# Optimization experiments

Measured on AMD Instinct MI355X. Metric: run time of the kernel, lower is better.

Reference implementation:

```python
import jax, jax.numpy as jnp
import numpy as np

B, S, E, H, L, NQ, FFN, V, C = 16, 2048, 256, 4, 2, 8, 512, 50257, 2
DK = E // H  # wires per attention head


def _pos_encoding(seq_len, dim):
    pos = jnp.arange(seq_len, dtype=jnp.float32)[:, None]
    div = jnp.exp(jnp.arange(0, dim, 2, dtype=jnp.float32) * (-np.log(10000.0) / dim))
    pe = jnp.zeros((seq_len, dim), dtype=jnp.float32)
    pe = pe.at[:, 0::2].set(jnp.sin(pos * div))
    pe = pe.at[:, 1::2].set(jnp.cos(pos * div))
    return pe


def _layernorm(x, g, b, eps=1e-5):
    m = x.mean(-1, keepdims=True)
    v = ((x - m) ** 2).mean(-1, keepdims=True)
    return (x - m) / jnp.sqrt(v + eps) * g + b


def setup_inputs() -> dict:
    key = jax.random.key(0)
    ks = jax.random.split(key, 9)
    f = lambda k, shape, s: jax.random.normal(k, shape, dtype=jnp.float32) * s
    return {
        "tokens": jax.random.randint(ks[0], (B, S), 0, V),
        "embed": f(ks[1], (V, E), 0.02),
        "attn_theta": f(ks[2], (L, DK), 1.0),
        "combine_w": f(ks[3], (L, E, E), 0.05),
        "combine_b": jnp.zeros((L, E), jnp.float32),
        "ffn_theta": f(ks[4], (L, NQ), 1.0),
        "lin1_w": f(ks[5], (L, NQ, FFN), 0.1),
        "lin1_b": jnp.zeros((L, FFN), jnp.float32),
        "lin2_w": f(ks[6], (L, FFN, E), 0.05),
        "lin2_b": jnp.zeros((L, E), jnp.float32),
        "ln1_g": jnp.ones((L, E), jnp.float32),
        "ln1_b": jnp.zeros((L, E), jnp.float32),
        "ln2_g": jnp.ones((L, E), jnp.float32),
        "ln2_b": jnp.zeros((L, E), jnp.float32),
        "cls_w": f(ks[7], (E, C), 0.05),
        "cls_b": jnp.zeros((C,), jnp.float32),
    }


def reference(tokens, embed, attn_theta, combine_w, combine_b, ffn_theta,
              lin1_w, lin1_b, lin2_w, lin2_b, ln1_g, ln1_b, ln2_g, ln2_b,
              cls_w, cls_b):
    # token embedding + sinusoidal positional encoding
    x = embed[tokens] + _pos_encoding(S, E)[None]  # [B,S,E]
    for l in range(L):
        # QuantumAttention: per-head RX-encode(x) then trainable RX(theta),
        # PauliZ expectation => cos(x + theta); same theta shared across heads,
        # head split/merge preserves feature layout => tile theta over heads.
        theta = jnp.tile(attn_theta[l], H)  # [E]
        attn = jnp.einsum('bse,ef->bsf', jnp.cos(x + theta), combine_w[l]) + combine_b[l]
        x = _layernorm(x + attn, ln1_g[l], ln1_b[l])
        # FeedForwardQuantum: RX-encode first NQ features, trainable RY(theta),
        # PauliZ expectation => cos(x) * cos(theta)
        q = jnp.cos(x[..., :NQ]) * jnp.cos(ffn_theta[l])  # [B,S,NQ]
        h = jax.nn.relu(jnp.einsum('bsn,nf->bsf', q, lin1_w[l]) + lin1_b[l])
        ffn = jnp.einsum('bsf,fe->bse', h, lin2_w[l]) + lin2_b[l]
        x = _layernorm(x + ffn, ln2_g[l], ln2_b[l])
    pooled = x.mean(axis=1)  # [B,E]
    return pooled @ cls_w + cls_b  # [B,C] logits
```

## Files before the change

kernel.cpp:

```cpp
#include <hip/hip_runtime.h>
#include <cstdint>
#include <cstddef>

#define SEQ   2048
#define EDIM  256
#define FFND  512
#define NBATCH 16
#define XLD   264

typedef unsigned short u16;
typedef __attribute__((ext_vector_type(8))) __bf16 bf16x8;
typedef __attribute__((ext_vector_type(4))) float f32x4;

__device__ __forceinline__ float bf2f(u16 u) {
  union { unsigned int w; float f; } v; v.w = ((unsigned int)u) << 16; return v.f;
}
__device__ __forceinline__ u16 f2bf(float f) {
  union { float f; unsigned int w; } v; v.f = f;
  unsigned int r = v.w + 0x7fffu + ((v.w >> 16) & 1u);
  return (u16)(r >> 16);
}
__device__ __forceinline__ float fast_cos(float x) {
  float r = x * 0.15915494309189535f;
  r = r - floorf(r);
  return __builtin_amdgcn_cosf(r);
}
__device__ __forceinline__ void unpack8(bf16x8 v, float* o) {
  const u16* p = (const u16*)&v;
  #pragma unroll
  for (int j = 0; j < 8; ++j) o[j] = bf2f(p[j]);
}

__global__ void sniff_kernel(const void* embed, int* flag) {
  int t = threadIdx.x;
  const u16* p = (const u16*)embed;
  int c = 0;
  #pragma unroll
  for (int j = 0; j < 8; ++j) {
    u16 v = p[t * 8 + j];
    int e = (v >> 7) & 0xff;
    c += (e > 128) ? 1 : 0;
  }
  #pragma unroll
  for (int d = 1; d < 64; d <<= 1) c += __shfl_xor(c, d);
  if (t == 0) *flag = (c > 64) ? 1 : 0;
}

struct CanonArgs { const void* p[14]; };

__global__ void canon_kernel(CanonArgs a, const int* __restrict__ flag, u16* __restrict__ dst) {
  const int off[15] = {0, 128, 131200, 131712, 131728, 139920, 140944, 403088,
                       403600, 404112, 404624, 405136, 405648, 406160, 406162};
  int i = blockIdx.x * 256 + threadIdx.x;
  if (i >= 406162) return;
  int isf32 = *flag;
  int s = 0;
  #pragma unroll
  for (int k = 0; k < 13; ++k) s += (i >= off[k + 1]) ? 1 : 0;
  int j = i - off[s];
  u16 v = isf32 ? f2bf(((const float*)a.p[s])[j]) : ((const u16*)a.p[s])[j];
  dst[i] = v;
}

__global__ void prep_kernel(const u16* __restrict__ cw, const u16* __restrict__ l2,
                            u16* __restrict__ cwT, u16* __restrict__ l2T) {
  int id = blockIdx.x * 256 + threadIdx.x;
  if (id < 2 * 256 * 256) {
    int l = id >> 16, rem = id & 65535;
    int kc = rem >> 11, n = (rem >> 3) & 255, kj = rem & 7;
    cwT[id] = cw[l * 65536 + (kc * 8 + kj) * 256 + n];
  } else {
    int j = id - 131072;
    if (j < 2 * 512 * 256) {
      int l = j >> 17, rem = j & 131071;
      int kc = rem >> 11, n = (rem >> 3) & 255, kj = rem & 7;
      l2T[j] = l2[l * 131072 + (kc * 8 + kj) * 256 + n];
    }
  }
}

__launch_bounds__(256, 2)
__global__ void mega_kernel(const int* __restrict__ tokens, const void* __restrict__ embed,
                            const int* __restrict__ flag, const u16* __restrict__ canon,
                            const u16* __restrict__ cwT, const u16* __restrict__ l2T,
                            float* __restrict__ pooled) {
  __shared__ u16 xt[64 * XLD];
  __shared__ union {
    struct { u16 Bt[256 * 64]; u16 At[64 * 64]; u16 qs[64 * 8]; } k;
    struct { float2 sstat[64][5]; float2 sms[64]; } ln;
  } sh;
  __shared__ u16 thL[64];

  const int tid = threadIdx.x;
  const int wave = tid >> 6, lane = tid & 63;
  const int fr = lane & 15, fq = lane >> 4;
  const int m0 = blockIdx.x * 64;
  const int isf32 = *flag;

  int cols[4];
  #pragma unroll
  for (int ni = 0; ni < 4; ++ni) cols[ni] = wave * 64 + ni * 16 + fr;

  {
    const float c0 = 9.210340371976184f / 128.f;
    const float inv2pi = 0.15915494309189535f;
    #pragma unroll
    for (int it = 0; it < 8; ++it) {
      int c = it * 256 + tid;
      int r = c >> 5, e8 = c & 31;
      int tok = tokens[m0 + r];
      float ev[8];
      if (isf32) {
        const float* ep = (const float*)embed + (size_t)tok * EDIM + e8 * 8;
        float4 a = *(const float4*)ep, b = *(const float4*)(ep + 4);
        ev[0]=a.x; ev[1]=a.y; ev[2]=a.z; ev[3]=a.w; ev[4]=b.x; ev[5]=b.y; ev[6]=b.z; ev[7]=b.w;
      } else {
        const u16* ep = (const u16*)embed + (size_t)tok * EDIM + e8 * 8;
        uint4 v = *(const uint4*)ep;
        unpack8(*(const bf16x8*)&v, ev);
      }
      int s = (m0 + r) & (SEQ - 1);
      u16 o[8];
      #pragma unroll
      for (int j = 0; j < 8; ++j) {
        int e = e8 * 8 + j, i = e >> 1;
        float rev = (float)s * (__expf(-(float)i * c0) * inv2pi);
        rev = rev - floorf(rev);
        float pe = (e & 1) ? __builtin_amdgcn_cosf(rev) : __builtin_amdgcn_sinf(rev);
        o[j] = f2bf(ev[j] + pe);
      }
      *(uint4*)(xt + r * XLD + e8 * 8) = *(const uint4*)o;
    }
  }
  __syncthreads();

  f32x4 acc[4][4];

  auto mfma_step = [&]() {
    const bf16x8* Av = (const bf16x8*)sh.k.At;
    const bf16x8* Bv = (const bf16x8*)sh.k.Bt;
    #pragma unroll
    for (int ks = 0; ks < 2; ++ks) {
      const int kc = ks * 4 + fq;
      bf16x8 af[4], bfv[4];
      #pragma unroll
      for (int mi = 0; mi < 4; ++mi) af[mi] = Av[kc * 64 + ((mi * 16 + fr) ^ kc)];
      #pragma unroll
      for (int ni = 0; ni < 4; ++ni) bfv[ni] = Bv[kc * 256 + cols[ni]];
      #pragma unroll
      for (int mi = 0; mi < 4; ++mi)
        #pragma unroll
        for (int ni = 0; ni < 4; ++ni)
          acc[mi][ni] = __builtin_amdgcn_mfma_f32_16x16x32_bf16(af[mi], bfv[ni], acc[mi][ni], 0, 0, 0);
    }
  };

  auto epilogue = [&](const u16* bias, const u16* gamma, const u16* beta) {
    float bcol[4];
    #pragma unroll
    for (int ni = 0; ni < 4; ++ni) bcol[ni] = bf2f(bias[cols[ni]]);
    #pragma unroll
    for (int mi = 0; mi < 4; ++mi)
      #pragma unroll
      for (int rg = 0; rg < 4; ++rg) {
        int lrow = mi * 16 + fq * 4 + rg;
        #pragma unroll
        for (int ni = 0; ni < 4; ++ni)
          acc[mi][ni][rg] += bf2f(xt[lrow * XLD + cols[ni]]) + bcol[ni];
      }
    float sr[4][4], sq[4][4];
    #pragma unroll
    for (int mi = 0; mi < 4; ++mi)
      #pragma unroll
      for (int rg = 0; rg < 4; ++rg) {
        float a = 0.f, b = 0.f;
        #pragma unroll
        for (int ni = 0; ni < 4; ++ni) { float t2 = acc[mi][ni][rg]; a += t2; b += t2 * t2; }
        sr[mi][rg] = a; sq[mi][rg] = b;
      }
    #pragma unroll
    for (int d = 1; d < 16; d <<= 1)
      #pragma unroll
      for (int mi = 0; mi < 4; ++mi)
        #pragma unroll
        for (int rg = 0; rg < 4; ++rg) {
          sr[mi][rg] += __shfl_xor(sr[mi][rg], d);
          sq[mi][rg] += __shfl_xor(sq[mi][rg], d);
        }
    if (fr == 0) {
      #pragma unroll
      for (int mi = 0; mi < 4; ++mi)
        #pragma unroll
        for (int rg = 0; rg < 4; ++rg)
          sh.ln.sstat[mi * 16 + fq * 4 + rg][wave] = float2{sr[mi][rg], sq[mi][rg]};
    }
    __syncthreads();
    if (tid < 64) {
      float s = 0.f, s2 = 0.f;
      #pragma unroll
      for (int w = 0; w < 4; ++w) { float2 p = sh.ln.sstat[tid][w]; s += p.x; s2 += p.y; }
      float mean = s * (1.f / 256.f);
      float var = fmaxf(s2 * (1.f / 256.f) - mean * mean, 0.f);
      sh.ln.sms[tid] = float2{mean, rsqrtf(var + 1e-5f)};
    }
    __syncthreads();
    float gcol[4], btc[4];
    #pragma unroll
    for (int ni = 0; ni < 4; ++ni) { gcol[ni] = bf2f(gamma[cols[ni]]); btc[ni] = bf2f(beta[cols[ni]]); }
    #pragma unroll
    for (int mi = 0; mi < 4; ++mi)
      #pragma unroll
      for (int rg = 0; rg < 4; ++rg) {
        int lrow = mi * 16 + fq * 4 + rg;
        float2 ms = sh.ln.sms[lrow];
        #pragma unroll
        for (int ni = 0; ni < 4; ++ni) {
          float o = (acc[mi][ni][rg] - ms.x) * ms.y * gcol[ni] + btc[ni];
          xt[lrow * XLD + cols[ni]] = f2bf(o);
        }
      }
    __syncthreads();
  };

  for (int l = 0; l < 2; ++l) {
    if (tid < 8) ((uint4*)thL)[tid] = ((const uint4*)(canon + l * 64))[tid];
    __syncthreads();
    #pragma unroll
    for (int i = 0; i < 4; ++i)
      #pragma unroll
      for (int j = 0; j < 4; ++j) acc[i][j] = {0.f, 0.f, 0.f, 0.f};
    {
      const u16* Bbase = cwT + l * 65536;
      for (int k0 = 0; k0 < 256; k0 += 64) {
        const u16* bsrc = Bbase + (k0 >> 3) * 2048;
        #pragma unroll
        for (int it = 0; it < 8; ++it) {
          int c = tid + it * 256;
          __builtin_amdgcn_global_load_lds(
              (const __attribute__((address_space(1))) void*)(bsrc + (size_t)c * 8),
              (__attribute__((address_space(3))) void*)(sh.k.Bt + c * 8), 16, 0, 0);
        }
        #pragma unroll
        for (int it = 0; it < 2; ++it) {
          int c = it * 256 + tid;
          int f8 = c >> 6, r = c & 63;
          uint4 g = *(const uint4*)(xt + r * XLD + k0 + f8 * 8);
          u16* gp = (u16*)&g;
          #pragma unroll
          for (int j = 0; j < 8; ++j)
            gp[j] = f2bf(fast_cos(bf2f(gp[j]) + bf2f(thL[f8 * 8 + j])));
          ((uint4*)sh.k.At)[f8 * 64 + (r ^ f8)] = g;
        }
        __syncthreads();
        mfma_step();
        __syncthreads();
      }
    }
    epilogue(canon + 131200 + l * 256, canon + 403600 + l * 256, canon + 404112 + l * 256);

    #pragma unroll
    for (int rep = 0; rep < 2; ++rep) {
      int idx = tid + rep * 256;
      int r = idx >> 3, n = idx & 7;
      float cth = fast_cos(bf2f(canon[131712 + l * 8 + n]));
      sh.k.qs[r * 8 + n] = f2bf(fast_cos(bf2f(xt[r * XLD + n])) * cth);
    }
    __syncthreads();

    #pragma unroll
    for (int i = 0; i < 4; ++i)
      #pragma unroll
      for (int j = 0; j < 4; ++j) acc[i][j] = {0.f, 0.f, 0.f, 0.f};
    {
      const u16* B2 = l2T + l * 131072;
      const u16* w1 = canon + 131728 + l * 4096;
      const u16* b1 = canon + 139920 + l * 512;
      for (int k0 = 0; k0 < 512; k0 += 64) {
        const u16* bsrc = B2 + (k0 >> 3) * 2048;
        #pragma unroll
        for (int it = 0; it < 8; ++it) {
          int c = tid + it * 256;
          __builtin_amdgcn_global_load_lds(
              (const __attribute__((address_space(1))) void*)(bsrc + (size_t)c * 8),
              (__attribute__((address_space(3))) void*)(sh.k.Bt + c * 8), 16, 0, 0);
        }
        #pragma unroll
        for (int it = 0; it < 2; ++it) {
          int c = it * 256 + tid;
          int kc = c >> 6, r = c & 63;
          int cc = (k0 >> 3) + kc;
          float qf[8], hv[8];
          unpack8(((const bf16x8*)sh.k.qs)[r], qf);
          { uint4 bv = *(const uint4*)(b1 + cc * 8); unpack8(*(const bf16x8*)&bv, hv); }
          #pragma unroll
          for (int n = 0; n < 8; ++n) {
            uint4 wv = *(const uint4*)(w1 + n * 512 + cc * 8);
            float wf[8];
            unpack8(*(const bf16x8*)&wv, wf);
            #pragma unroll
            for (int j = 0; j < 8; ++j) hv[j] += qf[n] * wf[j];
          }
          uint4 g; u16* gp = (u16*)&g;
          #pragma unroll
          for (int j = 0; j < 8; ++j) gp[j] = f2bf(fmaxf(hv[j], 0.f));
          ((uint4*)sh.k.At)[kc * 64 + (r ^ kc)] = g;
        }
        __syncthreads();
        mfma_step();
        __syncthreads();
      }
    }
    epilogue(canon + 403088 + l * 256, canon + 404624 + l * 256, canon + 405136 + l * 256);
  }

  {
    float s = 0.f;
    #pragma unroll 8
    for (int r = 0; r < 64; ++r) s += bf2f(xt[r * XLD + tid]);
    atomicAdd(&pooled[(m0 >> 11) * EDIM + tid], s);
  }
}

__global__ void logits_kernel(const float* __restrict__ pooled, const u16* __restrict__ clsw,
                              const u16* __restrict__ clsb, const int* __restrict__ flag,
                              void* __restrict__ out) {
  int t = threadIdx.x;
  int b = t >> 4, sub = t & 15;
  float a0 = 0.f, a1 = 0.f;
  #pragma unroll
  for (int j = 0; j < 16; ++j) {
    int e = sub * 16 + j;
    float p = pooled[b * 256 + e];
    a0 += p * bf2f(clsw[e * 2 + 0]);
    a1 += p * bf2f(clsw[e * 2 + 1]);
  }
  #pragma unroll
  for (int d = 1; d < 16; d <<= 1) {
    a0 += __shfl_xor(a0, d);
    a1 += __shfl_xor(a1, d);
  }
  if (sub == 0) {
    float o0 = a0 * (1.f / 2048.f) + bf2f(clsb[0]);
    float o1 = a1 * (1.f / 2048.f) + bf2f(clsb[1]);
    if (*flag) {
      ((float*)out)[b * 2 + 0] = o0; ((float*)out)[b * 2 + 1] = o1;
    } else {
      ((u16*)out)[b * 2 + 0] = f2bf(o0); ((u16*)out)[b * 2 + 1] = f2bf(o1);
    }
  }
}

extern "C" void kernel_launch(void* const* d_in, const int* in_sizes, int n_in,
                              void* d_out, int out_size, void* d_ws, size_t ws_size,
                              hipStream_t stream) {
  const int* tokens = (const int*)d_in[0];

  char* ws = (char*)d_ws;
  u16*   canon  = (u16*)(ws + 0);
  u16*   cwT    = (u16*)(ws + 1048576);
  u16*   l2T    = (u16*)(ws + 1310720);
  float* pooled = (float*)(ws + 1835008);
  int*   flag   = (int*)(ws + 1851392);

  sniff_kernel<<<1, 64, 0, stream>>>(d_in[1], flag);

  CanonArgs ca;
  for (int i = 0; i < 14; ++i) ca.p[i] = d_in[i + 2];
  canon_kernel<<<1587, 256, 0, stream>>>(ca, flag, canon);

  prep_kernel<<<1536, 256, 0, stream>>>(canon + 128, canon + 140944, cwT, l2T);

  hipMemsetAsync(pooled, 0, NBATCH * EDIM * sizeof(float), stream);

  mega_kernel<<<512, 256, 0, stream>>>(tokens, d_in[1], flag, canon, cwT, l2T, pooled);

  logits_kernel<<<1, 256, 0, stream>>>(pooled, canon + 405648, canon + 406160, flag, d_out);
}
```

Measured before the change: 215.4 us.

## Merge preprocessing kernels, inline dtype sniffing, use fp32 FFN weights and shared-memory LN stats

Removes the separate sniff and canon kernels. Each kernel now detects the input dtype inline, and a single prep kernel both canonicalizes the parameters and transposes the weights, cutting kernel launches and dependent passes. The FFN first layer now keeps its weights, bias and q values in fp32, which avoids bf16 unpacking in the hot loop. LayerNorm partial sums are written straight to shared memory, replacing the cross-lane shuffle reduction. The trade-offs are that every thread repeats the 128-word sniff read, there is more shared-memory traffic for the LN partials, and the fp32 weight loads are wider.

```diff
diff --git a/kernel.cpp b/kernel.cpp
--- a/kernel.cpp
+++ b/kernel.cpp
@@ -30,64 +30,64 @@
   #pragma unroll
   for (int j = 0; j < 8; ++j) o[j] = bf2f(p[j]);
 }
-
-__global__ void sniff_kernel(const void* embed, int* flag) {
-  int t = threadIdx.x;
-  const u16* p = (const u16*)embed;
+__device__ __forceinline__ int sniff128(const void* embed) {
+  const unsigned* p = (const unsigned*)embed;
   int c = 0;
   #pragma unroll
-  for (int j = 0; j < 8; ++j) {
-    u16 v = p[t * 8 + j];
-    int e = (v >> 7) & 0xff;
-    c += (e > 128) ? 1 : 0;
-  }
-  #pragma unroll
-  for (int d = 1; d < 64; d <<= 1) c += __shfl_xor(c, d);
-  if (t == 0) *flag = (c > 64) ? 1 : 0;
+  for (int j = 0; j < 128; ++j) {
+    unsigned v = p[j];
+    c += (((v >> 7) & 0xffu) > 128u) ? 1 : 0;
+    c += (((v >> 23) & 0xffu) > 128u) ? 1 : 0;
+  }
+  return c > 32;
+}
+__device__ __forceinline__ float cvt(const void* p, int j, int isf32) {
+  return isf32 ? ((const float*)p)[j] : bf2f(((const u16*)p)[j]);
 }
 
 struct CanonArgs { const void* p[14]; };
 
-__global__ void canon_kernel(CanonArgs a, const int* __restrict__ flag, u16* __restrict__ dst) {
-  const int off[15] = {0, 128, 131200, 131712, 131728, 139920, 140944, 403088,
-                       403600, 404112, 404624, 405136, 405648, 406160, 406162};
-  int i = blockIdx.x * 256 + threadIdx.x;
-  if (i >= 406162) return;
-  int isf32 = *flag;
-  int s = 0;
-  #pragma unroll
-  for (int k = 0; k < 13; ++k) s += (i >= off[k + 1]) ? 1 : 0;
-  int j = i - off[s];
-  u16 v = isf32 ? f2bf(((const float*)a.p[s])[j]) : ((const u16*)a.p[s])[j];
-  dst[i] = v;
-}
-
-__global__ void prep_kernel(const u16* __restrict__ cw, const u16* __restrict__ l2,
-                            u16* __restrict__ cwT, u16* __restrict__ l2T) {
+__global__ void prep_kernel(const void* __restrict__ emb, CanonArgs a,
+                            u16* __restrict__ canon, u16* __restrict__ cwT,
+                            u16* __restrict__ l2T, float* __restrict__ w1f,
+                            float* __restrict__ b1f) {
+  const int isf32 = sniff128(emb);
   int id = blockIdx.x * 256 + threadIdx.x;
-  if (id < 2 * 256 * 256) {
-    int l = id >> 16, rem = id & 65535;
+  if (id < 406162) {
+    const int off[15] = {0, 128, 131200, 131712, 131728, 139920, 140944, 403088,
+                         403600, 404112, 404624, 405136, 405648, 406160, 406162};
+    int s = 0;
+    #pragma unroll
+    for (int k = 0; k < 13; ++k) s += (id >= off[k + 1]) ? 1 : 0;
+    canon[id] = f2bf(cvt(a.p[s], id - off[s], isf32));
+  } else if (id < 537234) {
+    int j = id - 406162;
+    int l = j >> 16, rem = j & 65535;
     int kc = rem >> 11, n = (rem >> 3) & 255, kj = rem & 7;
-    cwT[id] = cw[l * 65536 + (kc * 8 + kj) * 256 + n];
-  } else {
-    int j = id - 131072;
-    if (j < 2 * 512 * 256) {
-      int l = j >> 17, rem = j & 131071;
-      int kc = rem >> 11, n = (rem >> 3) & 255, kj = rem & 7;
-      l2T[j] = l2[l * 131072 + (kc * 8 + kj) * 256 + n];
-    }
+    cwT[j] = f2bf(cvt(a.p[1], l * 65536 + (kc * 8 + kj) * 256 + n, isf32));
+  } else if (id < 799378) {
+    int j = id - 537234;
+    int l = j >> 17, rem = j & 131071;
+    int kc = rem >> 11, n = (rem >> 3) & 255, kj = rem & 7;
+    l2T[j] = f2bf(cvt(a.p[6], l * 131072 + (kc * 8 + kj) * 256 + n, isf32));
+  } else if (id < 807570) {
+    int j = id - 799378;
+    w1f[j] = cvt(a.p[4], j, isf32);
+  } else if (id < 808594) {
+    int j = id - 807570;
+    b1f[j] = cvt(a.p[5], j, isf32);
   }
 }
 
 __launch_bounds__(256, 2)
 __global__ void mega_kernel(const int* __restrict__ tokens, const void* __restrict__ embed,
-                            const int* __restrict__ flag, const u16* __restrict__ canon,
-                            const u16* __restrict__ cwT, const u16* __restrict__ l2T,
-                            float* __restrict__ pooled) {
+                            const u16* __restrict__ canon, const u16* __restrict__ cwT,
+                            const u16* __restrict__ l2T, const float* __restrict__ w1f,
+                            const float* __restrict__ b1f, float* __restrict__ pooled) {
   __shared__ u16 xt[64 * XLD];
   __shared__ union {
-    struct { u16 Bt[256 * 64]; u16 At[64 * 64]; u16 qs[64 * 8]; } k;
-    struct { float2 sstat[64][5]; float2 sms[64]; } ln;
+    struct { u16 Bt[256 * 64]; u16 At[64 * 64]; float qsf[64 * 8]; } k;
+    struct { float2 part[64][65]; float2 ms[64]; } ln;
   } sh;
   __shared__ u16 thL[64];
 
@@ -95,7 +95,7 @@
   const int wave = tid >> 6, lane = tid & 63;
   const int fr = lane & 15, fq = lane >> 4;
   const int m0 = blockIdx.x * 64;
-  const int isf32 = *flag;
+  const int isf32 = sniff128(embed);
 
   int cols[4];
   #pragma unroll
@@ -164,44 +164,26 @@
       #pragma unroll
       for (int rg = 0; rg < 4; ++rg) {
         int lrow = mi * 16 + fq * 4 + rg;
-        #pragma unroll
-        for (int ni = 0; ni < 4; ++ni)
-          acc[mi][ni][rg] += bf2f(xt[lrow * XLD + cols[ni]]) + bcol[ni];
-      }
-    float sr[4][4], sq[4][4];
-    #pragma unroll
-    for (int mi = 0; mi < 4; ++mi)
-      #pragma unroll
-      for (int rg = 0; rg < 4; ++rg) {
         float a = 0.f, b = 0.f;
         #pragma unroll
-        for (int ni = 0; ni < 4; ++ni) { float t2 = acc[mi][ni][rg]; a += t2; b += t2 * t2; }
-        sr[mi][rg] = a; sq[mi][rg] = b;
-      }
-    #pragma unroll
-    for (int d = 1; d < 16; d <<= 1)
-      #pragma unroll
-      for (int mi = 0; mi < 4; ++mi)
-        #pragma unroll
-        for (int rg = 0; rg < 4; ++rg) {
-          sr[mi][rg] += __shfl_xor(sr[mi][rg], d);
-          sq[mi][rg] += __shfl_xor(sq[mi][rg], d);
-        }
-    if (fr == 0) {
-      #pragma unroll
-      for (int mi = 0; mi < 4; ++mi)
-        #pragma unroll
-        for (int rg = 0; rg < 4; ++rg)
-          sh.ln.sstat[mi * 16 + fq * 4 + rg][wave] = float2{sr[mi][rg], sq[mi][rg]};
-    }
+        for (int ni = 0; ni < 4; ++ni) {
+          float t2 = acc[mi][ni][rg] + bf2f(xt[lrow * XLD + cols[ni]]) + bcol[ni];
+          acc[mi][ni][rg] = t2;
+          a += t2; b += t2 * t2;
+        }
+        sh.ln.part[lrow][wave * 16 + fr] = float2{a, b};
+      }
     __syncthreads();
     if (tid < 64) {
       float s = 0.f, s2 = 0.f;
       #pragma unroll
-      for (int w = 0; w < 4; ++w) { float2 p = sh.ln.sstat[tid][w]; s += p.x; s2 += p.y; }
+      for (int f = 0; f < 64; f += 2) {
+        float4 p = *(const float4*)&sh.ln.part[tid][f];
+        s += p.x + p.z; s2 += p.y + p.w;
+      }
       float mean = s * (1.f / 256.f);
       float var = fmaxf(s2 * (1.f / 256.f) - mean * mean, 0.f);
-      sh.ln.sms[tid] = float2{mean, rsqrtf(var + 1e-5f)};
+      sh.ln.ms[tid] = float2{mean, rsqrtf(var + 1e-5f)};
     }
     __syncthreads();
     float gcol[4], btc[4];
@@ -212,7 +194,7 @@
       #pragma unroll
       for (int rg = 0; rg < 4; ++rg) {
         int lrow = mi * 16 + fq * 4 + rg;
-        float2 ms = sh.ln.sms[lrow];
+        float2 ms = sh.ln.ms[lrow];
         #pragma unroll
         for (int ni = 0; ni < 4; ++ni) {
           float o = (acc[mi][ni][rg] - ms.x) * ms.y * gcol[ni] + btc[ni];
@@ -263,7 +245,7 @@
       int idx = tid + rep * 256;
       int r = idx >> 3, n = idx & 7;
       float cth = fast_cos(bf2f(canon[131712 + l * 8 + n]));
-      sh.k.qs[r * 8 + n] = f2bf(fast_cos(bf2f(xt[r * XLD + n])) * cth);
+      sh.k.qsf[r * 8 + n] = fast_cos(bf2f(xt[r * XLD + n])) * cth;
     }
     __syncthreads();
 
@@ -273,8 +255,8 @@
       for (int j = 0; j < 4; ++j) acc[i][j] = {0.f, 0.f, 0.f, 0.f};
     {
       const u16* B2 = l2T + l * 131072;
-      const u16* w1 = canon + 131728 + l * 4096;
-      const u16* b1 = canon + 139920 + l * 512;
+      const float* w1l = w1f + l * 4096;
+      const float* b1l = b1f + l * 512;
       for (int k0 = 0; k0 < 512; k0 += 64) {
         const u16* bsrc = B2 + (k0 >> 3) * 2048;
         #pragma unroll
@@ -289,16 +271,24 @@
           int c = it * 256 + tid;
           int kc = c >> 6, r = c & 63;
           int cc = (k0 >> 3) + kc;
-          float qf[8], hv[8];
-          unpack8(((const bf16x8*)sh.k.qs)[r], qf);
-          { uint4 bv = *(const uint4*)(b1 + cc * 8); unpack8(*(const bf16x8*)&bv, hv); }
+          float4 qa = *(const float4*)(sh.k.qsf + r * 8);
+          float4 qb = *(const float4*)(sh.k.qsf + r * 8 + 4);
+          float qv[8] = {qa.x, qa.y, qa.z, qa.w, qb.x, qb.y, qb.z, qb.w};
+          float hv[8];
+          {
+            float4 b0 = *(const float4*)(b1l + cc * 8);
+            float4 b1v = *(const float4*)(b1l + cc * 8 + 4);
+            hv[0]=b0.x; hv[1]=b0.y; hv[2]=b0.z; hv[3]=b0.w;
+            hv[4]=b1v.x; hv[5]=b1v.y; hv[6]=b1v.z; hv[7]=b1v.w;
+          }
           #pragma unroll
           for (int n = 0; n < 8; ++n) {
-            uint4 wv = *(const uint4*)(w1 + n * 512 + cc * 8);
-            float wf[8];
-            unpack8(*(const bf16x8*)&wv, wf);
-            #pragma unroll
-            for (int j = 0; j < 8; ++j) hv[j] += qf[n] * wf[j];
+            float4 w0 = *(const float4*)(w1l + n * 512 + cc * 8);
+            float4 w1v = *(const float4*)(w1l + n * 512 + cc * 8 + 4);
+            hv[0] += qv[n] * w0.x;  hv[1] += qv[n] * w0.y;
+            hv[2] += qv[n] * w0.z;  hv[3] += qv[n] * w0.w;
+            hv[4] += qv[n] * w1v.x; hv[5] += qv[n] * w1v.y;
+            hv[6] += qv[n] * w1v.z; hv[7] += qv[n] * w1v.w;
           }
           uint4 g; u16* gp = (u16*)&g;
           #pragma unroll
@@ -322,8 +312,9 @@
 }
 
 __global__ void logits_kernel(const float* __restrict__ pooled, const u16* __restrict__ clsw,
-                              const u16* __restrict__ clsb, const int* __restrict__ flag,
+                              const u16* __restrict__ clsb, const void* __restrict__ embed,
                               void* __restrict__ out) {
+  const int isf32 = sniff128(embed);
   int t = threadIdx.x;
   int b = t >> 4, sub = t & 15;
   float a0 = 0.f, a1 = 0.f;
@@ -342,7 +333,7 @@
   if (sub == 0) {
     float o0 = a0 * (1.f / 2048.f) + bf2f(clsb[0]);
     float o1 = a1 * (1.f / 2048.f) + bf2f(clsb[1]);
-    if (*flag) {
+    if (isf32) {
       ((float*)out)[b * 2 + 0] = o0; ((float*)out)[b * 2 + 1] = o1;
     } else {
       ((u16*)out)[b * 2 + 0] = f2bf(o0); ((u16*)out)[b * 2 + 1] = f2bf(o1);
@@ -359,20 +350,17 @@
   u16*   canon  = (u16*)(ws + 0);
   u16*   cwT    = (u16*)(ws + 1048576);
   u16*   l2T    = (u16*)(ws + 1310720);
-  float* pooled = (float*)(ws + 1835008);
-  int*   flag   = (int*)(ws + 1851392);
-
-  sniff_kernel<<<1, 64, 0, stream>>>(d_in[1], flag);
+  float* w1f    = (float*)(ws + 1835008);
+  float* b1f    = (float*)(ws + 1867776);
+  float* pooled = (float*)(ws + 1871872);
 
   CanonArgs ca;
   for (int i = 0; i < 14; ++i) ca.p[i] = d_in[i + 2];
-  canon_kernel<<<1587, 256, 0, stream>>>(ca, flag, canon);
-
-  prep_kernel<<<1536, 256, 0, stream>>>(canon + 128, canon + 140944, cwT, l2T);
-
+
+  prep_kernel<<<3159, 256, 0, stream>>>(d_in[1], ca, canon, cwT, l2T, w1f, b1f);
   hipMemsetAsync(pooled, 0, NBATCH * EDIM * sizeof(float), stream);
 
-  mega_kernel<<<512, 256, 0, stream>>>(tokens, d_in[1], flag, canon, cwT, l2T, pooled);
-
-  logits_kernel<<<1, 256, 0, stream>>>(pooled, canon + 405648, canon + 406160, flag, d_out);
-}
+  mega_kernel<<<512, 256, 0, stream>>>(tokens, d_in[1], canon, cwT, l2T, w1f, b1f, pooled);
+
+  logits_kernel<<<1, 256, 0, stream>>>(pooled, canon + 405648, canon + 406160, d_in[1], d_out);
+}
```

Result: slower. 230.1 us (+6.8%).
